# Kernel optimization log

Measured on AMD Instinct MI355X. Metric: run time of the kernel, lower is better.

The kernel has to match this reference:

```python
import jax, jax.numpy as jnp
import numpy as np

B, L, H, V = 32768, 24, 64, 64
EPS_NORM = 1e-12  # F.normalize eps
EPS_LN = 1e-5     # LayerNorm eps


def setup_inputs() -> dict:
    key = jax.random.key(0)
    ks = jax.random.split(key, 12)
    s = 1.0 / np.sqrt(H)
    init_val = float(np.log(0.9184 / (1.0 - 0.9184)))
    return {
        "seq": jax.random.randint(ks[0], (B, L), 0, V, dtype=jnp.int32),
        "embed": jax.random.normal(ks[1], (V, H), jnp.float32),
        "w1": jax.random.normal(ks[2], (H, 2 * H), jnp.float32) * s,
        "b1": jnp.zeros((2 * H,), jnp.float32),
        "w2": jax.random.normal(ks[3], (2 * H, H), jnp.float32) * s,
        "b2": jnp.zeros((H,), jnp.float32),
        "ln_g": jnp.ones((H,), jnp.float32),
        "ln_b": jnp.zeros((H,), jnp.float32),
        "rp_w": jax.random.normal(ks[4], (H, H), jnp.float32) * s,
        "rp_b": jnp.zeros((H,), jnp.float32),
        "out_w": jax.random.normal(ks[5], (H, V), jnp.float32) * s,
        "out_b": jnp.zeros((V,), jnp.float32),
        "alpha_logits": jnp.full((L,), init_val, jnp.float32),
    }


def _layernorm(x, g, b):
    mu = jnp.mean(x, axis=-1, keepdims=True)
    var = jnp.mean(jnp.square(x - mu), axis=-1, keepdims=True)
    return (x - mu) * jax.lax.rsqrt(var + EPS_LN) * g + b


def reference(seq, embed, w1, b1, w2, b2, ln_g, ln_b, rp_w, rp_b, out_w, out_b, alpha_logits):
    h = embed[seq]  # [B, L, H]
    ff = jax.nn.relu(h @ w1 + b1) @ w2 + b2
    h = _layernorm(h + ff, ln_g, ln_b)

    alphas = jax.nn.sigmoid(alpha_logits) * 0.49 + 0.5  # [L]
    ht = jnp.swapaxes(h[:, :-1, :], 0, 1)  # [L-1, B, H] time-major

    def step(M, inp):
        k, a = inp  # k: [B, H], a: scalar
        kn = k / jnp.maximum(jnp.linalg.norm(k, axis=-1, keepdims=True), EPS_NORM)
        vp = jnp.einsum('bij,bj->bi', M, kn)
        dv = k - vp
        M = M + (1.0 - a) * (dv[:, :, None] * kn[:, None, :])
        return M, None

    M0 = jnp.zeros((seq.shape[0], h.shape[-1], h.shape[-1]), h.dtype)
    M, _ = jax.lax.scan(step, M0, (ht, alphas[:-1]))

    v = jnp.einsum('bij,bj->bi', M, h[:, -1, :])
    return (v @ rp_w + rp_b) @ out_w + out_b  # [B, V]
```

## Files before the change

kernel.cpp:

```cpp
#include <hip/hip_runtime.h>
#include <hip/hip_bf16.h>
#include <math.h>

#define B_SZ 32768
#define L_SZ 24
#define H_SZ 64
#define V_SZ 64

#define KN_WS 0
#define WK_WS 4096
#define NRM_WS 8192
#define B2_WS 8256
#define CF_WS 8320
#define WS_F 8344

#define ROW 96
#define KN_L 0
#define WK_L 6144
#define TL_L 12288
#define LDS_F 12440

__global__ __launch_bounds__(64) void k_tab(
    const float* __restrict__ embed, const float* __restrict__ w1, const float* __restrict__ b1,
    const float* __restrict__ w2, const float* __restrict__ b2,
    const float* __restrict__ ln_g, const float* __restrict__ ln_b,
    const float* __restrict__ rp_w, const float* __restrict__ rp_b,
    const float* __restrict__ out_w, const float* __restrict__ out_b,
    const float* __restrict__ alpha_logits, float* __restrict__ ws)
{
  const int v = blockIdx.x;
  const int j = threadIdx.x;

  if (v < V_SZ) {
    const float ev = embed[v * H_SZ + j];
    float h0 = b1[j], h1 = b1[j + 64];
    #pragma unroll
    for (int k = 0; k < H_SZ; ++k) {
      const float ek = __shfl(ev, k);
      h0 = fmaf(ek, w1[k * 128 + j], h0);
      h1 = fmaf(ek, w1[k * 128 + 64 + j], h1);
    }
    h0 = fmaxf(h0, 0.0f);
    h1 = fmaxf(h1, 0.0f);
    float x = ev + b2[j];
    #pragma unroll
    for (int k = 0; k < H_SZ; ++k) {
      x = fmaf(__shfl(h0, k), w2[k * H_SZ + j], x);
      x = fmaf(__shfl(h1, k), w2[(k + 64) * H_SZ + j], x);
    }
    float mu = x;
    #pragma unroll
    for (int m = 1; m < 64; m <<= 1) mu += __shfl_xor(mu, m);
    mu *= (1.0f / 64.0f);
    const float dv = x - mu;
    float var = dv * dv;
    #pragma unroll
    for (int m = 1; m < 64; m <<= 1) var += __shfl_xor(var, m);
    var *= (1.0f / 64.0f);
    const float y = dv * rsqrtf(var + 1e-5f) * ln_g[j] + ln_b[j];
    float n2 = y * y;
    #pragma unroll
    for (int m = 1; m < 64; m <<= 1) n2 += __shfl_xor(n2, m);
    const float nrm = sqrtf(n2);
    const float rn = 1.0f / fmaxf(nrm, 1e-12f);
    ws[KN_WS + v * H_SZ + j] = y * rn;
    if (j == 0) ws[NRM_WS + v] = nrm;
    float t1 = 0.0f;
    #pragma unroll
    for (int k = 0; k < H_SZ; ++k) t1 = fmaf(__shfl(y, k), rp_w[k * H_SZ + j], t1);
    float wk = 0.0f;
    #pragma unroll
    for (int k = 0; k < H_SZ; ++k) wk = fmaf(__shfl(t1, k), out_w[k * V_SZ + j], wk);
    ws[WK_WS + v * H_SZ + j] = wk;
  } else {
    float s = out_b[j];
    #pragma unroll
    for (int k = 0; k < H_SZ; ++k) s = fmaf(rp_b[k], out_w[k * V_SZ + j], s);
    ws[B2_WS + j] = s;
    if (j < L_SZ) {
      float cf = 0.0f;
      if (j < L_SZ - 1) {
        const float a = 1.0f / (1.0f + expf(-alpha_logits[j])) * 0.49f + 0.5f;
        cf = 1.0f - a;
      }
      ws[CF_WS + j] = cf;
    }
  }
}

__global__ __launch_bounds__(256) void k_scan(
    const int* __restrict__ seq, const float* __restrict__ ws, float* __restrict__ out)
{
  __shared__ float lds[LDS_F];
  const int tid = threadIdx.x;
  const float4* ws4 = (const float4*)ws;

  for (int i = tid; i < 2048; i += 256) {
    const float4 f = ws4[i];
    float* base = (i & 1024) ? (lds + WK_L) : (lds + KN_L);
    const int r = (i >> 4) & 63;
    const int c = (i & 15) * 4;
    *(float4*)(base + r * ROW + 12 * (c >> 3) + (c & 7)) = f;
  }
  for (int i = tid; i < 38; i += 256)
    *(((float4*)(lds + TL_L)) + i) = ws4[2048 + i];
  __syncthreads();

  const float* knL = lds + KN_L;
  const float* wkL = lds + WK_L;
  const float* nrmL = lds + TL_L;
  const float* b2L = lds + TL_L + 64;
  const float* cfL = lds + TL_L + 128;

  const int lane = tid & 63;
  const int wv = tid >> 6;
  const int g = lane >> 3;
  const int s = lane & 7;
  const int batch = blockIdx.x * 32 + wv * 8 + g;
  const int cb = 12 * s;

  int sqv[L_SZ];
  const int4* sp = (const int4*)(seq + batch * L_SZ);
  #pragma unroll
  for (int i = 0; i < 6; ++i) ((int4*)sqv)[i] = sp[i];

  float qh[8], oa[8];
  {
    const int tok = sqv[L_SZ - 1];
    const float nv = nrmL[tok];
    const float* qr = knL + tok * ROW + cb;
    const float4 a = *(const float4*)qr;
    const float4 b = *(const float4*)(qr + 4);
    qh[0] = a.x * nv; qh[1] = a.y * nv; qh[2] = a.z * nv; qh[3] = a.w * nv;
    qh[4] = b.x * nv; qh[5] = b.y * nv; qh[6] = b.z * nv; qh[7] = b.w * nv;
  }
  #pragma unroll
  for (int i = 0; i < 8; ++i) oa[i] = 0.0f;

  #pragma unroll
  for (int t = L_SZ - 2; t >= 0; --t) {
    const int tok = sqv[t];
    const float* kr = knL + tok * ROW + cb;
    const float4 ka = *(const float4*)kr;
    const float4 kb = *(const float4*)(kr + 4);
    float kv[8] = {ka.x, ka.y, ka.z, ka.w, kb.x, kb.y, kb.z, kb.w};

    float p = 0.0f;
    #pragma unroll
    for (int i = 0; i < 8; ++i) p = fmaf(kv[i], qh[i], p);
    p += __shfl_xor(p, 1);
    p += __shfl_xor(p, 2);
    p += __shfl_xor(p, 4);

    const float c = cfL[t] * p;

    #pragma unroll
    for (int i = 0; i < 8; ++i) qh[i] = fmaf(-c, kv[i], qh[i]);

    const float* wr = wkL + tok * ROW + cb;
    const float4 wa = *(const float4*)wr;
    const float4 wb = *(const float4*)(wr + 4);
    oa[0] = fmaf(c, wa.x, oa[0]); oa[1] = fmaf(c, wa.y, oa[1]);
    oa[2] = fmaf(c, wa.z, oa[2]); oa[3] = fmaf(c, wa.w, oa[3]);
    oa[4] = fmaf(c, wb.x, oa[4]); oa[5] = fmaf(c, wb.y, oa[5]);
    oa[6] = fmaf(c, wb.z, oa[6]); oa[7] = fmaf(c, wb.w, oa[7]);
  }

  #pragma unroll
  for (int i = 0; i < 8; ++i) oa[i] += b2L[s * 8 + i];

  float4* op = (float4*)(out + batch * V_SZ + s * 8);
  op[0] = make_float4(oa[0], oa[1], oa[2], oa[3]);
  op[1] = make_float4(oa[4], oa[5], oa[6], oa[7]);
}

extern "C" void kernel_launch(void* const* d_in, const int* in_sizes, int n_in,
                              void* d_out, int out_size, void* d_ws, size_t ws_size,
                              hipStream_t stream)
{
  const int*   seq          = (const int*)d_in[0];
  const float* embed        = (const float*)d_in[1];
  const float* w1           = (const float*)d_in[2];
  const float* b1           = (const float*)d_in[3];
  const float* w2           = (const float*)d_in[4];
  const float* b2           = (const float*)d_in[5];
  const float* ln_g         = (const float*)d_in[6];
  const float* ln_b         = (const float*)d_in[7];
  const float* rp_w         = (const float*)d_in[8];
  const float* rp_b         = (const float*)d_in[9];
  const float* out_w        = (const float*)d_in[10];
  const float* out_b        = (const float*)d_in[11];
  const float* alpha_logits = (const float*)d_in[12];
  float* ws   = (float*)d_ws;
  float* outp = (float*)d_out;

  hipLaunchKernelGGL(k_tab, dim3(V_SZ + 1), dim3(64), 0, stream,
                     embed, w1, b1, w2, b2, ln_g, ln_b,
                     rp_w, rp_b, out_w, out_b, alpha_logits, ws);
  hipLaunchKernelGGL(k_scan, dim3(B_SZ / 32), dim3(256), 0, stream,
                     seq, ws, outp);
}
```

Baseline: 29.00 us.

## Precompute Gram matrix of normalized keys and solve scan coefficients in scalar form

Adds a kernel that builds the 64x64 Gram matrix of normalized token keys. The scan then computes the per-step coefficients with a scalar triangular recurrence over Gram entries instead of updating a 64-wide query vector with shuffle reductions. Output accumulation becomes a separate pass over those coefficients, and each block now covers 64 batches. The cost is an extra kernel launch, O(L^2) scalar work per batch done by only 16 lanes per wave (low utilization), and more LDS.

```diff
diff --git a/kernel.cpp b/kernel.cpp
--- a/kernel.cpp
+++ b/kernel.cpp
@@ -12,13 +12,16 @@
 #define NRM_WS 8192
 #define B2_WS 8256
 #define CF_WS 8320
-#define WS_F 8344
+#define G_WS  8384
+#define WS_F  12480
 
 #define ROW 96
-#define KN_L 0
-#define WK_L 6144
-#define TL_L 12288
-#define LDS_F 12440
+#define G_L   0
+#define WK_L  4096
+#define NRM_L 10240
+#define CB_L  10304
+#define TO_L  11840
+#define LDS_F 13376
 
 __global__ __launch_bounds__(64) void k_tab(
     const float* __restrict__ embed, const float* __restrict__ w1, const float* __restrict__ b1,
@@ -88,6 +91,24 @@
   }
 }
 
+__global__ __launch_bounds__(64) void k_gram(float* __restrict__ ws)
+{
+  const int u = blockIdx.x;
+  const int j = threadIdx.x;
+  const float a = ws[KN_WS + u * H_SZ + j];
+  float r[64];
+  const float4* rp = (const float4*)(ws + KN_WS + j * H_SZ);
+  #pragma unroll
+  for (int i = 0; i < 16; ++i) {
+    const float4 f = rp[i];
+    r[4 * i] = f.x; r[4 * i + 1] = f.y; r[4 * i + 2] = f.z; r[4 * i + 3] = f.w;
+  }
+  float s = 0.0f;
+  #pragma unroll
+  for (int k = 0; k < 64; ++k) s = fmaf(__shfl(a, k), r[k], s);
+  ws[G_WS + u * H_SZ + j] = s;
+}
+
 __global__ __launch_bounds__(256) void k_scan(
     const int* __restrict__ seq, const float* __restrict__ ws, float* __restrict__ out)
 {
@@ -95,83 +116,94 @@
   const int tid = threadIdx.x;
   const float4* ws4 = (const float4*)ws;
 
-  for (int i = tid; i < 2048; i += 256) {
-    const float4 f = ws4[i];
-    float* base = (i & 1024) ? (lds + WK_L) : (lds + KN_L);
-    const int r = (i >> 4) & 63;
+  for (int i = tid; i < 1024; i += 256)
+    ((float4*)(lds + G_L))[i] = ws4[G_WS / 4 + i];
+  for (int i = tid; i < 1024; i += 256) {
+    const float4 f = ws4[WK_WS / 4 + i];
+    const int r = i >> 4;
     const int c = (i & 15) * 4;
-    *(float4*)(base + r * ROW + 12 * (c >> 3) + (c & 7)) = f;
-  }
-  for (int i = tid; i < 38; i += 256)
-    *(((float4*)(lds + TL_L)) + i) = ws4[2048 + i];
+    *(float4*)(lds + WK_L + r * ROW + 12 * (c >> 3) + (c & 7)) = f;
+  }
+  if (tid < 16) ((float4*)(lds + NRM_L))[tid] = ws4[NRM_WS / 4 + tid];
   __syncthreads();
-
-  const float* knL = lds + KN_L;
-  const float* wkL = lds + WK_L;
-  const float* nrmL = lds + TL_L;
-  const float* b2L = lds + TL_L + 64;
-  const float* cfL = lds + TL_L + 128;
 
   const int lane = tid & 63;
   const int wv = tid >> 6;
-  const int g = lane >> 3;
-  const int s = lane & 7;
-  const int batch = blockIdx.x * 32 + wv * 8 + g;
-  const int cb = 12 * s;
-
-  int sqv[L_SZ];
-  const int4* sp = (const int4*)(seq + batch * L_SZ);
+  const float* cfg = ws + CF_WS;
+
+  if (lane < 16) {
+    const int ab = wv * 16 + lane;
+    const int batch = blockIdx.x * 64 + ab;
+    int g[24];
+    const int4* sp = (const int4*)(seq + batch * L_SZ);
+    #pragma unroll
+    for (int i = 0; i < 6; ++i) {
+      const int4 t4 = sp[i];
+      g[4 * i] = t4.x; g[4 * i + 1] = t4.y; g[4 * i + 2] = t4.z; g[4 * i + 3] = t4.w;
+    }
+    int* tob = (int*)lds + TO_L + ab * 24;
+    #pragma unroll
+    for (int i = 0; i < 6; ++i)
+      ((int4*)tob)[i] = make_int4(g[4 * i] * ROW, g[4 * i + 1] * ROW,
+                                  g[4 * i + 2] * ROW, g[4 * i + 3] * ROW);
+    const int q = g[23];
+    const float nl = lds[NRM_L + q];
+    const float* Gt = lds + G_L;
+    float* cb = lds + CB_L + ab * 24;
+    float P[23];
+    #pragma unroll
+    for (int t = 0; t < 23; ++t) P[t] = 0.0f;
+    #pragma unroll
+    for (int s = 22; s >= 0; --s) {
+      const float base = nl * Gt[(g[s] << 6) + q];
+      const float cs = cfg[s] * (base - P[s]);
+      cb[s] = cs;
+      #pragma unroll
+      for (int t = 0; t < s; ++t)
+        P[t] = fmaf(cs, Gt[(g[t] << 6) + g[s]], P[t]);
+    }
+    cb[23] = 0.0f;
+  }
+  __syncthreads();
+
+  const int grp = lane >> 3;
+  const int s8 = lane & 7;
+  const int cbse = 12 * s8;
+  const float* wkL = lds + WK_L;
+  const float* b2g = ws + B2_WS + s8 * 8;
+  const float4 bA = *(const float4*)(b2g);
+  const float4 bB = *(const float4*)(b2g + 4);
+
   #pragma unroll
-  for (int i = 0; i < 6; ++i) ((int4*)sqv)[i] = sp[i];
-
-  float qh[8], oa[8];
-  {
-    const int tok = sqv[L_SZ - 1];
-    const float nv = nrmL[tok];
-    const float* qr = knL + tok * ROW + cb;
-    const float4 a = *(const float4*)qr;
-    const float4 b = *(const float4*)(qr + 4);
-    qh[0] = a.x * nv; qh[1] = a.y * nv; qh[2] = a.z * nv; qh[3] = a.w * nv;
-    qh[4] = b.x * nv; qh[5] = b.y * nv; qh[6] = b.z * nv; qh[7] = b.w * nv;
-  }
-  #pragma unroll
-  for (int i = 0; i < 8; ++i) oa[i] = 0.0f;
-
-  #pragma unroll
-  for (int t = L_SZ - 2; t >= 0; --t) {
-    const int tok = sqv[t];
-    const float* kr = knL + tok * ROW + cb;
-    const float4 ka = *(const float4*)kr;
-    const float4 kb = *(const float4*)(kr + 4);
-    float kv[8] = {ka.x, ka.y, ka.z, ka.w, kb.x, kb.y, kb.z, kb.w};
-
-    float p = 0.0f;
-    #pragma unroll
-    for (int i = 0; i < 8; ++i) p = fmaf(kv[i], qh[i], p);
-    p += __shfl_xor(p, 1);
-    p += __shfl_xor(p, 2);
-    p += __shfl_xor(p, 4);
-
-    const float c = cfL[t] * p;
-
-    #pragma unroll
-    for (int i = 0; i < 8; ++i) qh[i] = fmaf(-c, kv[i], qh[i]);
-
-    const float* wr = wkL + tok * ROW + cb;
-    const float4 wa = *(const float4*)wr;
-    const float4 wb = *(const float4*)(wr + 4);
-    oa[0] = fmaf(c, wa.x, oa[0]); oa[1] = fmaf(c, wa.y, oa[1]);
-    oa[2] = fmaf(c, wa.z, oa[2]); oa[3] = fmaf(c, wa.w, oa[3]);
-    oa[4] = fmaf(c, wb.x, oa[4]); oa[5] = fmaf(c, wb.y, oa[5]);
-    oa[6] = fmaf(c, wb.z, oa[6]); oa[7] = fmaf(c, wb.w, oa[7]);
-  }
-
-  #pragma unroll
-  for (int i = 0; i < 8; ++i) oa[i] += b2L[s * 8 + i];
-
-  float4* op = (float4*)(out + batch * V_SZ + s * 8);
-  op[0] = make_float4(oa[0], oa[1], oa[2], oa[3]);
-  op[1] = make_float4(oa[4], oa[5], oa[6], oa[7]);
+  for (int it = 0; it < 2; ++it) {
+    const int ab = wv * 16 + it * 8 + grp;
+    const int batch = blockIdx.x * 64 + ab;
+    float cv[24]; int tv[24];
+    const float4* cp = (const float4*)(lds + CB_L + ab * 24);
+    const int4* tp = (const int4*)((const int*)lds + TO_L + ab * 24);
+    #pragma unroll
+    for (int i = 0; i < 6; ++i) {
+      const float4 f = cp[i];
+      cv[4 * i] = f.x; cv[4 * i + 1] = f.y; cv[4 * i + 2] = f.z; cv[4 * i + 3] = f.w;
+      const int4 t4 = tp[i];
+      tv[4 * i] = t4.x; tv[4 * i + 1] = t4.y; tv[4 * i + 2] = t4.z; tv[4 * i + 3] = t4.w;
+    }
+    float oa[8] = {bA.x, bA.y, bA.z, bA.w, bB.x, bB.y, bB.z, bB.w};
+    #pragma unroll
+    for (int t = 0; t < 23; ++t) {
+      const float c = cv[t];
+      const float* wr = wkL + tv[t] + cbse;
+      const float4 wa = *(const float4*)wr;
+      const float4 wb = *(const float4*)(wr + 4);
+      oa[0] = fmaf(c, wa.x, oa[0]); oa[1] = fmaf(c, wa.y, oa[1]);
+      oa[2] = fmaf(c, wa.z, oa[2]); oa[3] = fmaf(c, wa.w, oa[3]);
+      oa[4] = fmaf(c, wb.x, oa[4]); oa[5] = fmaf(c, wb.y, oa[5]);
+      oa[6] = fmaf(c, wb.z, oa[6]); oa[7] = fmaf(c, wb.w, oa[7]);
+    }
+    float4* op = (float4*)(out + batch * V_SZ + s8 * 8);
+    op[0] = make_float4(oa[0], oa[1], oa[2], oa[3]);
+    op[1] = make_float4(oa[4], oa[5], oa[6], oa[7]);
+  }
 }
 
 extern "C" void kernel_launch(void* const* d_in, const int* in_sizes, int n_in,
@@ -197,6 +229,7 @@
   hipLaunchKernelGGL(k_tab, dim3(V_SZ + 1), dim3(64), 0, stream,
                      embed, w1, b1, w2, b2, ln_g, ln_b,
                      rp_w, rp_b, out_w, out_b, alpha_logits, ws);
-  hipLaunchKernelGGL(k_scan, dim3(B_SZ / 32), dim3(256), 0, stream,
+  hipLaunchKernelGGL(k_gram, dim3(V_SZ), dim3(64), 0, stream, ws);
+  hipLaunchKernelGGL(k_scan, dim3(B_SZ / 64), dim3(256), 0, stream,
                      seq, ws, outp);
 }
```

New measurement: 27.84 us. -4.0%, faster.
